# Kernel tuning notes

Measured on AMD Instinct MI355X. Metric: run time of the kernel, lower is better.

The kernel has to match this reference:

```python
import jax, jax.numpy as jnp
import numpy as np

B, S, H, V = 256, 15, 512, 50257

def setup_inputs() -> dict:
    key = jax.random.key(0)
    ks = jax.random.split(key, 12)
    sc_h = 1.0 / np.sqrt(H)
    sc_in = 1.0 / np.sqrt(2 * H)
    return {
        "input_tokens": jax.random.randint(ks[0], (B, 1), 0, V),
        "hidden": jax.random.normal(ks[1], (1, B, H), jnp.float32),
        "encoder_outputs": jax.random.normal(ks[2], (B, S, H), jnp.float32),
        "emb_table": jax.random.normal(ks[3], (V, H), jnp.float32),
        "attn_W": jax.random.uniform(ks[4], (H, H), jnp.float32, -sc_h, sc_h),
        "attn_b": jax.random.uniform(ks[5], (H,), jnp.float32, -sc_h, sc_h),
        "W_ih": jax.random.uniform(ks[6], (3 * H, 2 * H), jnp.float32, -sc_in, sc_in),
        "W_hh": jax.random.uniform(ks[7], (3 * H, H), jnp.float32, -sc_h, sc_h),
        "b_ih": jax.random.uniform(ks[8], (3 * H,), jnp.float32, -sc_h, sc_h),
        "b_hh": jax.random.uniform(ks[9], (3 * H,), jnp.float32, -sc_h, sc_h),
        "out_W": jax.random.uniform(ks[10], (V, H), jnp.float32, -sc_h, sc_h),
        "out_b": jax.random.uniform(ks[11], (V,), jnp.float32, -sc_h, sc_h),
    }


def reference(input_tokens, hidden, encoder_outputs, emb_table, attn_W, attn_b,
              W_ih, W_hh, b_ih, b_hh, out_W, out_b):
    # Embedding (dropout is identity in eval/reference mode): [B,1,H]
    embedded = emb_table[input_tokens]
    h = hidden[0]  # [B,H]

    # Bahdanau-style scores, vectorized over the seq dim instead of the python loop:
    # energies[b,s] = attn(enc[b,s]);  score[b,s] = <h[b], energies[b,s]>
    energies = jnp.einsum("bsh,oh->bso", encoder_outputs, attn_W) + attn_b  # [B,S,H]
    attn_scores = jnp.einsum("bso,bo->bs", energies, h)                      # [B,S]
    attn_weights = jax.nn.softmax(attn_scores, axis=1)                       # [B,S]

    # context = weights @ encoder_outputs: [B,1,H]
    context = jnp.einsum("bs,bsh->bh", attn_weights, encoder_outputs)[:, None, :]

    # GRU single step (PyTorch gate order: r, z, n)
    x = jnp.concatenate([embedded, context], axis=2)[:, 0]  # [B,2H]
    gi = x @ W_ih.T + b_ih   # [B,3H]
    gh = h @ W_hh.T + b_hh   # [B,3H]
    i_r, i_z, i_n = jnp.split(gi, 3, axis=1)
    h_r, h_z, h_n = jnp.split(gh, 3, axis=1)
    r = jax.nn.sigmoid(i_r + h_r)
    z = jax.nn.sigmoid(i_z + h_z)
    n = jnp.tanh(i_n + r * h_n)
    h_new = (1.0 - z) * n + z * h            # [B,H]

    logits = h_new[:, None, :] @ out_W.T + out_b   # [B,1,V]
    log_probs = jax.nn.log_softmax(logits, axis=-1)
    return log_probs, h_new[None], attn_weights
```

## Files before the change

### kernel.cpp

```cpp
#include <hip/hip_runtime.h>

#define V_SIZE 50257
#define B_SIZE 256
#define S_LEN  15
#define H_DIM  512
#define NBLK_LG 786

typedef __attribute__((ext_vector_type(8))) short bf16x8;
typedef __attribute__((ext_vector_type(4))) float f32x4;

__device__ __forceinline__ unsigned short f2bf(float f) {
    unsigned int u = __float_as_uint(f);
    u += 0x7fffu + ((u >> 16) & 1u);
    return (unsigned short)(u >> 16);
}

__global__ __launch_bounds__(256) void u_kernel(
    const float* __restrict__ hidden, const float* __restrict__ attn_W,
    float* __restrict__ u)
{
    __shared__ float h_s[16][H_DIM];
    const int tid = threadIdx.x;
    const int b0 = blockIdx.y * 16, n0 = blockIdx.x * 32;
    const float4* hv = (const float4*)(hidden + (size_t)b0 * H_DIM);
    float4* hs4 = (float4*)&h_s[0][0];
    #pragma unroll
    for (int i = 0; i < 8; ++i) hs4[tid + i * 256] = hv[tid + i * 256];
    __syncthreads();
    const int n = n0 + (tid & 31);
    const int m = (tid >> 5) * 2;
    float a0 = 0.f, a1 = 0.f;
    #pragma unroll 8
    for (int o = 0; o < H_DIM; ++o) {
        float w = attn_W[(size_t)o * H_DIM + n];
        a0 += h_s[m][o] * w;
        a1 += h_s[m + 1][o] * w;
    }
    u[(size_t)(b0 + m) * H_DIM + n] = a0;
    u[(size_t)(b0 + m + 1) * H_DIM + n] = a1;
}

__global__ __launch_bounds__(256) void attn_kernel(
    const float* __restrict__ hidden, const float* __restrict__ enc,
    const float* __restrict__ u, const int* __restrict__ tokens,
    const float* __restrict__ emb, float* __restrict__ attnw_out,
    unsigned short* __restrict__ x_bf, unsigned short* __restrict__ h_bf)
{
    const int b = blockIdx.x, tid = threadIdx.x;
    __shared__ float e_s[S_LEN][H_DIM];
    __shared__ float u_s[H_DIM];
    __shared__ float sc_s[S_LEN];
    __shared__ float w_s[S_LEN];
    {
        const float4* ev = (const float4*)(enc + (size_t)b * S_LEN * H_DIM);
        float4* es4 = (float4*)&e_s[0][0];
        #pragma unroll
        for (int i = 0; i < 8; ++i) {
            int idx = i * 256 + tid;
            if (idx < S_LEN * H_DIM / 4) es4[idx] = ev[idx];
        }
    }
    u_s[tid]       = u[(size_t)b * H_DIM + tid];
    u_s[tid + 256] = u[(size_t)b * H_DIM + tid + 256];
    h_bf[(size_t)b * H_DIM + tid]       = f2bf(hidden[(size_t)b * H_DIM + tid]);
    h_bf[(size_t)b * H_DIM + tid + 256] = f2bf(hidden[(size_t)b * H_DIM + tid + 256]);
    const int tok = tokens[b];
    x_bf[(size_t)b * 2 * H_DIM + tid]       = f2bf(emb[(size_t)tok * H_DIM + tid]);
    x_bf[(size_t)b * 2 * H_DIM + tid + 256] = f2bf(emb[(size_t)tok * H_DIM + tid + 256]);
    __syncthreads();
    const int wave = tid >> 6, lane = tid & 63;
    for (int s = wave; s < S_LEN; s += 4) {
        float acc = 0.f;
        #pragma unroll
        for (int k = 0; k < H_DIM / 64; ++k)
            acc += e_s[s][lane + k * 64] * u_s[lane + k * 64];
        #pragma unroll
        for (int off = 32; off; off >>= 1) acc += __shfl_down(acc, off);
        if (lane == 0) sc_s[s] = acc;
    }
    __syncthreads();
    float mx = -1e30f;
    for (int s = 0; s < S_LEN; ++s) mx = fmaxf(mx, sc_s[s]);
    float sum = 0.f;
    for (int s = 0; s < S_LEN; ++s) sum += __expf(sc_s[s] - mx);
    const float inv = 1.f / sum;
    if (tid < S_LEN) {
        float w = __expf(sc_s[tid] - mx) * inv;
        w_s[tid] = w;
        attnw_out[b * S_LEN + tid] = w;
    }
    __syncthreads();
    #pragma unroll
    for (int hh = 0; hh < 2; ++hh) {
        int h = tid + hh * 256;
        float c = 0.f;
        #pragma unroll
        for (int s = 0; s < S_LEN; ++s)
            c += w_s[s] * e_s[s][h];
        x_bf[(size_t)b * 2 * H_DIM + H_DIM + h] = f2bf(c);
    }
}

struct GemmP {
    const unsigned short* A; const float* B; const float* bias; float* C;
    int N; int K;
};

template<int BM, int BN, int BK, int WR, int WC>
__global__ __launch_bounds__(256) void gemm_nt(GemmP p0, GemmP p1)
{
    GemmP p = (blockIdx.z == 0) ? p0 : p1;
    constexpr int LDA = BK + 8;
    __shared__ __align__(16) unsigned short As[BM][LDA];
    __shared__ __align__(16) unsigned short Bs[BN][LDA];
    const int tid = threadIdx.x;
    const int bn0 = blockIdx.x * BN;
    const int bm0 = blockIdx.y * BM;
    const int wave = tid >> 6, lane = tid & 63;
    const int wm = (wave / WC) * (BM / WR);
    const int wn = (wave % WC) * (BN / WC);
    constexpr int MF = BM / WR / 16, NF = BN / WC / 16;
    const int n16 = lane & 15, quad = lane >> 4;

    f32x4 acc[MF][NF] = {};

    for (int k0 = 0; k0 < p.K; k0 += BK) {
        #pragma unroll
        for (int it = 0; it < BM / 32; ++it) {
            int v = it * 256 + tid;
            int row = v >> 3, seg = v & 7;
            *(uint4*)&As[row][seg * 8] =
                *(const uint4*)(p.A + (size_t)(bm0 + row) * p.K + k0 + seg * 8);
        }
        #pragma unroll
        for (int it = 0; it < BN / 32; ++it) {
            int v = it * 256 + tid;
            int row = v >> 3, seg = v & 7;
            int gv = bn0 + row;
            float4 w0 = make_float4(0, 0, 0, 0), w1 = make_float4(0, 0, 0, 0);
            if (gv < p.N) {
                const float4* src = (const float4*)(p.B + (size_t)gv * p.K + k0 + seg * 8);
                w0 = src[0]; w1 = src[1];
            }
            uint4 pk;
            pk.x = (unsigned)f2bf(w0.x) | ((unsigned)f2bf(w0.y) << 16);
            pk.y = (unsigned)f2bf(w0.z) | ((unsigned)f2bf(w0.w) << 16);
            pk.z = (unsigned)f2bf(w1.x) | ((unsigned)f2bf(w1.y) << 16);
            pk.w = (unsigned)f2bf(w1.z) | ((unsigned)f2bf(w1.w) << 16);
            *(uint4*)&Bs[row][seg * 8] = pk;
        }
        __syncthreads();
        #pragma unroll
        for (int kk = 0; kk < BK; kk += 32) {
            bf16x8 af[MF], bfr[NF];
            #pragma unroll
            for (int i = 0; i < MF; ++i)
                af[i] = *(const bf16x8*)&As[wm + i * 16 + n16][kk + quad * 8];
            #pragma unroll
            for (int j = 0; j < NF; ++j)
                bfr[j] = *(const bf16x8*)&Bs[wn + j * 16 + n16][kk + quad * 8];
            #pragma unroll
            for (int i = 0; i < MF; ++i)
                #pragma unroll
                for (int j = 0; j < NF; ++j)
                    acc[i][j] = __builtin_amdgcn_mfma_f32_16x16x32_bf16(
                        af[i], bfr[j], acc[i][j], 0, 0, 0);
        }
        __syncthreads();
    }
    #pragma unroll
    for (int i = 0; i < MF; ++i) {
        const int r0 = bm0 + wm + i * 16 + quad * 4;
        #pragma unroll
        for (int j = 0; j < NF; ++j) {
            const int c = bn0 + wn + j * 16 + n16;
            if (c < p.N) {
                const float bv = p.bias[c];
                #pragma unroll
                for (int r = 0; r < 4; ++r)
                    p.C[(size_t)(r0 + r) * p.N + c] = acc[i][j][r] + bv;
            }
        }
    }
}

template<bool PART>
__global__ __launch_bounds__(256, 2) void gemm_lg(
    const unsigned short* __restrict__ A, const float* __restrict__ B,
    const float* __restrict__ bias, float* __restrict__ C,
    float* __restrict__ pm, float* __restrict__ ps)
{
    constexpr int BN = 64;
    __shared__ __align__(16) unsigned short Bs[BN][H_DIM];
    const int tid = threadIdx.x;
    const int bn0 = blockIdx.x * BN;
    const int wave = tid >> 6, lane = tid & 63;
    const int wm = wave * 64;
    const int n16 = lane & 15, quad = lane >> 4;
    const int sx = n16 & 7;

    f32x4 acc[4][4] = {};
    const unsigned short* arow[4];
    #pragma unroll
    for (int i = 0; i < 4; ++i) arow[i] = A + (size_t)(wm + i * 16 + n16) * H_DIM;

    #pragma unroll
    for (int it = 0; it < 16; ++it) {
        int v = it * 256 + tid;
        int row = v >> 6, seg = v & 63;
        int gv = bn0 + row;
        float4 w0 = make_float4(0, 0, 0, 0), w1 = make_float4(0, 0, 0, 0);
        if (gv < V_SIZE) {
            const float4* src = (const float4*)(B + (size_t)gv * H_DIM + seg * 8);
            w0 = src[0]; w1 = src[1];
        }
        uint4 pk;
        pk.x = (unsigned)f2bf(w0.x) | ((unsigned)f2bf(w0.y) << 16);
        pk.y = (unsigned)f2bf(w0.z) | ((unsigned)f2bf(w0.w) << 16);
        pk.z = (unsigned)f2bf(w1.x) | ((unsigned)f2bf(w1.y) << 16);
        pk.w = (unsigned)f2bf(w1.z) | ((unsigned)f2bf(w1.w) << 16);
        *(uint4*)&Bs[row][(seg ^ (row & 7)) * 8] = pk;
    }
    __syncthreads();

    #pragma unroll 4
    for (int kk = 0; kk < H_DIM; kk += 32) {
        const int su = ((kk >> 3) + quad) ^ sx;
        bf16x8 af[4], bfr[4];
        #pragma unroll
        for (int i = 0; i < 4; ++i)
            af[i] = *(const bf16x8*)(arow[i] + kk + quad * 8);
        #pragma unroll
        for (int j = 0; j < 4; ++j)
            bfr[j] = *(const bf16x8*)&Bs[j * 16 + n16][su * 8];
        #pragma unroll
        for (int i = 0; i < 4; ++i)
            #pragma unroll
            for (int j = 0; j < 4; ++j)
                acc[i][j] = __builtin_amdgcn_mfma_f32_16x16x32_bf16(
                    af[i], bfr[j], acc[i][j], 0, 0, 0);
    }

    int cj[4]; float bvv[4]; bool okj[4];
    #pragma unroll
    for (int j = 0; j < 4; ++j) {
        cj[j] = bn0 + j * 16 + n16;
        okj[j] = cj[j] < V_SIZE;
        bvv[j] = okj[j] ? bias[cj[j]] : 0.f;
    }
    #pragma unroll
    for (int i = 0; i < 4; ++i) {
        const int r0 = wm + i * 16 + quad * 4;
        if (PART) {
            #pragma unroll
            for (int r = 0; r < 4; ++r) {
                float m = -1e30f;
                #pragma unroll
                for (int j = 0; j < 4; ++j)
                    if (okj[j]) m = fmaxf(m, acc[i][j][r] + bvv[j]);
                #pragma unroll
                for (int d = 1; d < 16; d <<= 1) m = fmaxf(m, __shfl_xor(m, d));
                float s = 0.f;
                #pragma unroll
                for (int j = 0; j < 4; ++j)
                    if (okj[j]) s += __expf(acc[i][j][r] + bvv[j] - m);
                #pragma unroll
                for (int d = 1; d < 16; d <<= 1) s += __shfl_xor(s, d);
                if (n16 == 0) {
                    pm[(size_t)blockIdx.x * B_SIZE + r0 + r] = m;
                    ps[(size_t)blockIdx.x * B_SIZE + r0 + r] = s;
                }
            }
        }
        #pragma unroll
        for (int j = 0; j < 4; ++j) if (okj[j]) {
            #pragma unroll
            for (int r = 0; r < 4; ++r)
                C[(size_t)(r0 + r) * V_SIZE + cj[j]] = acc[i][j][r] + bvv[j];
        }
    }
}

__global__ __launch_bounds__(256) void gru_kernel(
    const float* __restrict__ gi, const float* __restrict__ gh,
    const float* __restrict__ hidden, float* __restrict__ hnew_out,
    unsigned short* __restrict__ hnew_bf)
{
    const int idx = blockIdx.x * 256 + threadIdx.x;
    const int b = idx >> 9, h = idx & 511;
    const float* gib = gi + (size_t)b * 3 * H_DIM;
    const float* ghb = gh + (size_t)b * 3 * H_DIM;
    float r = 1.f / (1.f + __expf(-(gib[h] + ghb[h])));
    float z = 1.f / (1.f + __expf(-(gib[H_DIM + h] + ghb[H_DIM + h])));
    float n = gib[2 * H_DIM + h] + r * ghb[2 * H_DIM + h];
    n = 1.f - 2.f / (1.f + __expf(2.f * n));
    float hp = hidden[idx];
    float hn = (1.f - z) * n + z * hp;
    hnew_out[idx] = hn;
    hnew_bf[idx] = f2bf(hn);
}

__global__ __launch_bounds__(1024) void finalize_kernel(
    float* __restrict__ logits, const float* __restrict__ pm,
    const float* __restrict__ ps)
{
    const int b = blockIdx.x, tid = threadIdx.x;
    float m = -1e30f, s = 0.f;
    for (int i = tid; i < NBLK_LG; i += 1024) {
        float mm = pm[(size_t)i * B_SIZE + b], ss = ps[(size_t)i * B_SIZE + b];
        float nm = fmaxf(m, mm);
        s = s * __expf(m - nm) + ss * __expf(mm - nm);
        m = nm;
    }
    const int lane = tid & 63, wave = tid >> 6;
    #pragma unroll
    for (int off = 32; off; off >>= 1) {
        float m2 = __shfl_down(m, off), s2 = __shfl_down(s, off);
        float nm = fmaxf(m, m2);
        s = s * __expf(m - nm) + s2 * __expf(m2 - nm);
        m = nm;
    }
    __shared__ float msh[16], ssh[16], lse_sh;
    if (lane == 0) { msh[wave] = m; ssh[wave] = s; }
    __syncthreads();
    if (tid == 0) {
        float M = msh[0], S = ssh[0];
        for (int w = 1; w < 16; ++w) {
            float nm = fmaxf(M, msh[w]);
            S = S * __expf(M - nm) + ssh[w] * __expf(msh[w] - nm);
            M = nm;
        }
        lse_sh = M + logf(S);
    }
    __syncthreads();
    const float lse = lse_sh;
    constexpr int HALF = 25132;
    const int start = blockIdx.y * HALF;
    const int end = min(V_SIZE, start + HALF);
    float* p0 = logits + (size_t)b * V_SIZE + start;
    const int n = end - start;
    const int mis = (int)(((uintptr_t)p0 >> 2) & 3);
    int pre = mis ? (4 - mis) : 0; if (pre > n) pre = n;
    if (tid < pre) p0[tid] -= lse;
    const int nvec = (n - pre) >> 2;
    float4* rv = (float4*)(p0 + pre);
    for (int i = tid; i < nvec; i += 1024) {
        float4 v = rv[i];
        v.x -= lse; v.y -= lse; v.z -= lse; v.w -= lse;
        rv[i] = v;
    }
    const int rem = n - pre - (nvec << 2);
    if (tid < rem) p0[pre + (nvec << 2) + tid] -= lse;
}

__global__ __launch_bounds__(1024) void logsoftmax_kernel(float* __restrict__ logits)
{
    const int b = blockIdx.x, tid = threadIdx.x;
    float* row = logits + (size_t)b * V_SIZE;
    float m = -1e30f, s = 0.f;
    for (int c = tid; c < V_SIZE; c += 1024) {
        float x = row[c];
        float nm = fmaxf(m, x);
        s = s * __expf(m - nm) + __expf(x - nm);
        m = nm;
    }
    const int lane = tid & 63, wave = tid >> 6;
    #pragma unroll
    for (int off = 32; off; off >>= 1) {
        float m2 = __shfl_down(m, off), s2 = __shfl_down(s, off);
        float nm = fmaxf(m, m2);
        s = s * __expf(m - nm) + s2 * __expf(m2 - nm);
        m = nm;
    }
    __shared__ float msh[16], ssh[16], lse_sh;
    if (lane == 0) { msh[wave] = m; ssh[wave] = s; }
    __syncthreads();
    if (tid == 0) {
        float M = msh[0], S = ssh[0];
        for (int w = 1; w < 16; ++w) {
            float nm = fmaxf(M, msh[w]);
            S = S * __expf(M - nm) + ssh[w] * __expf(msh[w] - nm);
            M = nm;
        }
        lse_sh = M + logf(S);
    }
    __syncthreads();
    const float lse = lse_sh;
    for (int c = tid; c < V_SIZE; c += 1024) row[c] -= lse;
}

constexpr size_t OFF_U      = 0;
constexpr size_t OFF_XBF    = 524288;
constexpr size_t OFF_HBF    = 1048576;
constexpr size_t OFF_HNEWBF = 1310720;
constexpr size_t OFF_GI     = 1572864;
constexpr size_t OFF_GH     = 3145728;
constexpr size_t OFF_PM     = 4718592;
constexpr size_t OFF_PS     = 5523456;
constexpr size_t WS_NEED    = 6328320;

extern "C" void kernel_launch(void* const* d_in, const int* in_sizes, int n_in,
                              void* d_out, int out_size, void* d_ws, size_t ws_size,
                              hipStream_t stream) {
    const int*   tokens = (const int*)d_in[0];
    const float* hidden = (const float*)d_in[1];
    const float* enc    = (const float*)d_in[2];
    const float* emb    = (const float*)d_in[3];
    const float* attn_W = (const float*)d_in[4];
    const float* W_ih   = (const float*)d_in[6];
    const float* W_hh   = (const float*)d_in[7];
    const float* b_ih   = (const float*)d_in[8];
    const float* b_hh   = (const float*)d_in[9];
    const float* out_W  = (const float*)d_in[10];
    const float* out_b  = (const float*)d_in[11];

    float* out = (float*)d_out;
    float* logp      = out;
    float* hnew_out  = out + (size_t)B_SIZE * V_SIZE;
    float* attnw_out = hnew_out + (size_t)B_SIZE * H_DIM;

    char* ws = (char*)d_ws;
    float*          u_ws    = (float*)(ws + OFF_U);
    unsigned short* x_bf    = (unsigned short*)(ws + OFF_XBF);
    unsigned short* h_bf    = (unsigned short*)(ws + OFF_HBF);
    unsigned short* hnew_bf = (unsigned short*)(ws + OFF_HNEWBF);
    float*          gi_ws   = (float*)(ws + OFF_GI);
    float*          gh_ws   = (float*)(ws + OFF_GH);
    float*          pm_ws   = (float*)(ws + OFF_PM);
    float*          ps_ws   = (float*)(ws + OFF_PS);

    u_kernel<<<dim3(16, 16), 256, 0, stream>>>(hidden, attn_W, u_ws);
    attn_kernel<<<dim3(256), 256, 0, stream>>>(hidden, enc, u_ws, tokens, emb,
                                               attnw_out, x_bf, h_bf);
    GemmP gi_p { x_bf, W_ih, b_ih, gi_ws, 3 * H_DIM, 2 * H_DIM };
    GemmP gh_p { h_bf, W_hh, b_hh, gh_ws, 3 * H_DIM, H_DIM };
    gemm_nt<64, 64, 64, 2, 2><<<dim3(24, 4, 2), 256, 0, stream>>>(gi_p, gh_p);
    gru_kernel<<<dim3(512), 256, 0, stream>>>(gi_ws, gh_ws, hidden, hnew_out, hnew_bf);

    if (ws_size >= WS_NEED) {
        gemm_lg<true><<<dim3(NBLK_LG), 256, 0, stream>>>(
            hnew_bf, out_W, out_b, logp, pm_ws, ps_ws);
        finalize_kernel<<<dim3(256, 2), 1024, 0, stream>>>(logp, pm_ws, ps_ws);
    } else {
        gemm_lg<false><<<dim3(NBLK_LG), 256, 0, stream>>>(
            hnew_bf, out_W, out_b, logp, nullptr, nullptr);
        logsoftmax_kernel<<<dim3(256), 1024, 0, stream>>>(logp);
    }
}
```

Before: 379.1 us.

## Split output GEMM into K-tiled, half-M blocks with grouped rasterization

The vocabulary projection GEMM now uses 128-row M tiles instead of covering all 256 batch rows in one block. The weight tile is staged through a 64x136 shared buffer in four K steps rather than holding the full K=512 slice. Block indices are remapped so that the two M halves of each group of 8 N tiles run close together, which should let the second half read the fp32 weights from L2. The smaller shared footprint and raised launch bound allow more resident blocks and twice as many blocks overall. The cost is redundant weight loads and bf16 conversion per N tile, plus extra barriers per K step.

```diff
diff --git a/kernel.cpp b/kernel.cpp
--- a/kernel.cpp
+++ b/kernel.cpp
@@ -185,60 +185,67 @@
 }
 
 template<bool PART>
-__global__ __launch_bounds__(256, 2) void gemm_lg(
+__global__ __launch_bounds__(256, 4) void gemm_lg(
     const unsigned short* __restrict__ A, const float* __restrict__ B,
     const float* __restrict__ bias, float* __restrict__ C,
     float* __restrict__ pm, float* __restrict__ ps)
 {
-    constexpr int BN = 64;
-    __shared__ __align__(16) unsigned short Bs[BN][H_DIM];
+    constexpr int BN = 64, BK = 128;
+    constexpr int LDB = BK + 8;
+    __shared__ __align__(16) unsigned short Bs[BN][LDB];
     const int tid = threadIdx.x;
-    const int bn0 = blockIdx.x * BN;
+    const int blk = blockIdx.x;
+    int bx, by;
+    if (blk < 1568) { int g = blk >> 4, s = blk & 15; bx = g * 8 + (s & 7); by = s >> 3; }
+    else            { int s = blk - 1568;             bx = 784 + (s >> 1);  by = s & 1;  }
+    const int bn0 = bx * BN;
+    const int m0  = by * 128;
     const int wave = tid >> 6, lane = tid & 63;
-    const int wm = wave * 64;
+    const int wm = wave * 32;
     const int n16 = lane & 15, quad = lane >> 4;
-    const int sx = n16 & 7;
-
-    f32x4 acc[4][4] = {};
-    const unsigned short* arow[4];
-    #pragma unroll
-    for (int i = 0; i < 4; ++i) arow[i] = A + (size_t)(wm + i * 16 + n16) * H_DIM;
-
-    #pragma unroll
-    for (int it = 0; it < 16; ++it) {
-        int v = it * 256 + tid;
-        int row = v >> 6, seg = v & 63;
-        int gv = bn0 + row;
-        float4 w0 = make_float4(0, 0, 0, 0), w1 = make_float4(0, 0, 0, 0);
-        if (gv < V_SIZE) {
-            const float4* src = (const float4*)(B + (size_t)gv * H_DIM + seg * 8);
-            w0 = src[0]; w1 = src[1];
-        }
-        uint4 pk;
-        pk.x = (unsigned)f2bf(w0.x) | ((unsigned)f2bf(w0.y) << 16);
-        pk.y = (unsigned)f2bf(w0.z) | ((unsigned)f2bf(w0.w) << 16);
-        pk.z = (unsigned)f2bf(w1.x) | ((unsigned)f2bf(w1.y) << 16);
-        pk.w = (unsigned)f2bf(w1.z) | ((unsigned)f2bf(w1.w) << 16);
-        *(uint4*)&Bs[row][(seg ^ (row & 7)) * 8] = pk;
-    }
-    __syncthreads();
-
-    #pragma unroll 4
-    for (int kk = 0; kk < H_DIM; kk += 32) {
-        const int su = ((kk >> 3) + quad) ^ sx;
-        bf16x8 af[4], bfr[4];
-        #pragma unroll
-        for (int i = 0; i < 4; ++i)
-            af[i] = *(const bf16x8*)(arow[i] + kk + quad * 8);
-        #pragma unroll
-        for (int j = 0; j < 4; ++j)
-            bfr[j] = *(const bf16x8*)&Bs[j * 16 + n16][su * 8];
-        #pragma unroll
-        for (int i = 0; i < 4; ++i)
+
+    f32x4 acc[2][4] = {};
+    const unsigned short* arow[2];
+    #pragma unroll
+    for (int i = 0; i < 2; ++i)
+        arow[i] = A + (size_t)(m0 + wm + i * 16 + n16) * H_DIM;
+
+    for (int k0 = 0; k0 < H_DIM; k0 += BK) {
+        #pragma unroll
+        for (int it = 0; it < 4; ++it) {
+            int v = it * 256 + tid;
+            int row = v >> 4, seg = v & 15;
+            int gv = bn0 + row;
+            float4 w0 = make_float4(0, 0, 0, 0), w1 = make_float4(0, 0, 0, 0);
+            if (gv < V_SIZE) {
+                const float4* src = (const float4*)(B + (size_t)gv * H_DIM + k0 + seg * 8);
+                w0 = src[0]; w1 = src[1];
+            }
+            uint4 pk;
+            pk.x = (unsigned)f2bf(w0.x) | ((unsigned)f2bf(w0.y) << 16);
+            pk.y = (unsigned)f2bf(w0.z) | ((unsigned)f2bf(w0.w) << 16);
+            pk.z = (unsigned)f2bf(w1.x) | ((unsigned)f2bf(w1.y) << 16);
+            pk.w = (unsigned)f2bf(w1.z) | ((unsigned)f2bf(w1.w) << 16);
+            *(uint4*)&Bs[row][seg * 8] = pk;
+        }
+        __syncthreads();
+        #pragma unroll
+        for (int kk = 0; kk < BK; kk += 32) {
+            bf16x8 af[2], bfr[4];
+            #pragma unroll
+            for (int i = 0; i < 2; ++i)
+                af[i] = *(const bf16x8*)(arow[i] + k0 + kk + quad * 8);
             #pragma unroll
             for (int j = 0; j < 4; ++j)
-                acc[i][j] = __builtin_amdgcn_mfma_f32_16x16x32_bf16(
-                    af[i], bfr[j], acc[i][j], 0, 0, 0);
+                bfr[j] = *(const bf16x8*)&Bs[j * 16 + n16][kk + quad * 8];
+            #pragma unroll
+            for (int i = 0; i < 2; ++i)
+                #pragma unroll
+                for (int j = 0; j < 4; ++j)
+                    acc[i][j] = __builtin_amdgcn_mfma_f32_16x16x32_bf16(
+                        af[i], bfr[j], acc[i][j], 0, 0, 0);
+        }
+        __syncthreads();
     }
 
     int cj[4]; float bvv[4]; bool okj[4];
@@ -249,7 +256,7 @@
         bvv[j] = okj[j] ? bias[cj[j]] : 0.f;
     }
     #pragma unroll
-    for (int i = 0; i < 4; ++i) {
+    for (int i = 0; i < 2; ++i) {
         const int r0 = wm + i * 16 + quad * 4;
         if (PART) {
             #pragma unroll
@@ -267,8 +274,8 @@
                 #pragma unroll
                 for (int d = 1; d < 16; d <<= 1) s += __shfl_xor(s, d);
                 if (n16 == 0) {
-                    pm[(size_t)blockIdx.x * B_SIZE + r0 + r] = m;
-                    ps[(size_t)blockIdx.x * B_SIZE + r0 + r] = s;
+                    pm[(size_t)bx * B_SIZE + m0 + r0 + r] = m;
+                    ps[(size_t)bx * B_SIZE + m0 + r0 + r] = s;
                 }
             }
         }
@@ -276,7 +283,7 @@
         for (int j = 0; j < 4; ++j) if (okj[j]) {
             #pragma unroll
             for (int r = 0; r < 4; ++r)
-                C[(size_t)(r0 + r) * V_SIZE + cj[j]] = acc[i][j][r] + bvv[j];
+                C[(size_t)(m0 + r0 + r) * V_SIZE + cj[j]] = acc[i][j][r] + bvv[j];
         }
     }
 }
@@ -438,11 +445,11 @@
     gru_kernel<<<dim3(512), 256, 0, stream>>>(gi_ws, gh_ws, hidden, hnew_out, hnew_bf);
 
     if (ws_size >= WS_NEED) {
-        gemm_lg<true><<<dim3(NBLK_LG), 256, 0, stream>>>(
+        gemm_lg<true><<<dim3(2 * NBLK_LG), 256, 0, stream>>>(
             hnew_bf, out_W, out_b, logp, pm_ws, ps_ws);
         finalize_kernel<<<dim3(256, 2), 1024, 0, stream>>>(logp, pm_ws, ps_ws);
     } else {
-        gemm_lg<false><<<dim3(NBLK_LG), 256, 0, stream>>>(
+        gemm_lg<false><<<dim3(2 * NBLK_LG), 256, 0, stream>>>(
             hnew_bf, out_W, out_b, logp, nullptr, nullptr);
         logsoftmax_kernel<<<dim3(256), 1024, 0, stream>>>(logp);
     }
```

After: 366.1 us. 3.4% less time.

## Load output-projection weights directly from global into MFMA fragments, dropping LDS staging

Applied to the files above, without the earlier changes.

The logits GEMM no longer stages each 64-row slice of out_W as bf16 in shared memory behind a block barrier. Each wave now loads its B fragments straight from global memory inside the k-loop and converts fp32 to bf16 in registers. The launch-bounds occupancy hint rises from 2 to 3 blocks per CU. This removes the LDS footprint and the __syncthreads, letting weight loads overlap with MFMA work. In exchange, all four waves in a block fetch and convert the same weight tile, which multiplies cache traffic and conversion ALU work by four.

```diff
diff --git a/kernel.cpp b/kernel.cpp
--- a/kernel.cpp
+++ b/kernel.cpp
@@ -185,54 +185,50 @@
 }
 
 template<bool PART>
-__global__ __launch_bounds__(256, 2) void gemm_lg(
+__global__ __launch_bounds__(256, 3) void gemm_lg(
     const unsigned short* __restrict__ A, const float* __restrict__ B,
     const float* __restrict__ bias, float* __restrict__ C,
     float* __restrict__ pm, float* __restrict__ ps)
 {
     constexpr int BN = 64;
-    __shared__ __align__(16) unsigned short Bs[BN][H_DIM];
     const int tid = threadIdx.x;
     const int bn0 = blockIdx.x * BN;
     const int wave = tid >> 6, lane = tid & 63;
     const int wm = wave * 64;
     const int n16 = lane & 15, quad = lane >> 4;
-    const int sx = n16 & 7;
 
     f32x4 acc[4][4] = {};
     const unsigned short* arow[4];
     #pragma unroll
-    for (int i = 0; i < 4; ++i) arow[i] = A + (size_t)(wm + i * 16 + n16) * H_DIM;
-
-    #pragma unroll
-    for (int it = 0; it < 16; ++it) {
-        int v = it * 256 + tid;
-        int row = v >> 6, seg = v & 63;
-        int gv = bn0 + row;
-        float4 w0 = make_float4(0, 0, 0, 0), w1 = make_float4(0, 0, 0, 0);
-        if (gv < V_SIZE) {
-            const float4* src = (const float4*)(B + (size_t)gv * H_DIM + seg * 8);
-            w0 = src[0]; w1 = src[1];
-        }
-        uint4 pk;
-        pk.x = (unsigned)f2bf(w0.x) | ((unsigned)f2bf(w0.y) << 16);
-        pk.y = (unsigned)f2bf(w0.z) | ((unsigned)f2bf(w0.w) << 16);
-        pk.z = (unsigned)f2bf(w1.x) | ((unsigned)f2bf(w1.y) << 16);
-        pk.w = (unsigned)f2bf(w1.z) | ((unsigned)f2bf(w1.w) << 16);
-        *(uint4*)&Bs[row][(seg ^ (row & 7)) * 8] = pk;
-    }
-    __syncthreads();
+    for (int i = 0; i < 4; ++i)
+        arow[i] = A + (size_t)(wm + i * 16 + n16) * H_DIM;
+
+    const float* brow[4];
+    bool okj[4];
+    #pragma unroll
+    for (int j = 0; j < 4; ++j) {
+        int gv = bn0 + j * 16 + n16;
+        okj[j] = gv < V_SIZE;
+        brow[j] = B + (size_t)(okj[j] ? gv : 0) * H_DIM;
+    }
 
     #pragma unroll 4
     for (int kk = 0; kk < H_DIM; kk += 32) {
-        const int su = ((kk >> 3) + quad) ^ sx;
         bf16x8 af[4], bfr[4];
         #pragma unroll
         for (int i = 0; i < 4; ++i)
             af[i] = *(const bf16x8*)(arow[i] + kk + quad * 8);
         #pragma unroll
-        for (int j = 0; j < 4; ++j)
-            bfr[j] = *(const bf16x8*)&Bs[j * 16 + n16][su * 8];
+        for (int j = 0; j < 4; ++j) {
+            const float4* src = (const float4*)(brow[j] + kk + quad * 8);
+            float4 w0 = src[0], w1 = src[1];
+            union { uint4 u; bf16x8 v; } cv;
+            cv.u.x = (unsigned)f2bf(w0.x) | ((unsigned)f2bf(w0.y) << 16);
+            cv.u.y = (unsigned)f2bf(w0.z) | ((unsigned)f2bf(w0.w) << 16);
+            cv.u.z = (unsigned)f2bf(w1.x) | ((unsigned)f2bf(w1.y) << 16);
+            cv.u.w = (unsigned)f2bf(w1.z) | ((unsigned)f2bf(w1.w) << 16);
+            bfr[j] = cv.v;
+        }
         #pragma unroll
         for (int i = 0; i < 4; ++i)
             #pragma unroll
@@ -241,11 +237,10 @@
                     af[i], bfr[j], acc[i][j], 0, 0, 0);
     }
 
-    int cj[4]; float bvv[4]; bool okj[4];
+    int cj[4]; float bvv[4];
     #pragma unroll
     for (int j = 0; j < 4; ++j) {
         cj[j] = bn0 + j * 16 + n16;
-        okj[j] = cj[j] < V_SIZE;
         bvv[j] = okj[j] ? bias[cj[j]] : 0.f;
     }
     #pragma unroll
```

Result: slower. 429.7 us (+13.3%).
